# Performance work log

Measured on AMD Instinct MI355X. Metric: run time of the kernel, lower is better.

The kernel has to match this reference:

```python
import jax, jax.numpy as jnp
import numpy as np

S, B, D, H = 2048, 8, 512, 8
HD = D // H

def setup_inputs() -> dict:
    key = jax.random.key(0)
    ks = jax.random.split(key, 5)
    return {
        "src": jax.random.normal(ks[0], (S, B, D), dtype=jnp.float32),
        "in_proj_w": jax.random.normal(ks[1], (3 * D, D), dtype=jnp.float32) * (D ** -0.5),
        "in_proj_b": jax.random.normal(ks[2], (3 * D,), dtype=jnp.float32) * 0.02,
        "out_w": jax.random.normal(ks[3], (D, D), dtype=jnp.float32) * (D ** -0.5),
        "out_b": jax.random.normal(ks[4], (D,), dtype=jnp.float32) * 0.02,
    }

def reference(src, in_proj_w, in_proj_b, out_w, out_b):
    s, b, d = src.shape
    h, hd = H, HD
    # packed qkv projection: [S,B,3D]
    qkv = src @ in_proj_w.T + in_proj_b
    q, k, v = jnp.split(qkv, 3, axis=-1)
    # [S,B,H,hd]
    q = q.reshape(s, b, h, hd) * (hd ** -0.5)
    k = k.reshape(s, b, h, hd)
    v = v.reshape(s, b, h, hd)
    # scores [B,H,S,S]
    scores = jnp.einsum("sbhd,tbhd->bhst", q, k)
    attn = jax.nn.softmax(scores, axis=-1)
    # context [S,B,D]
    ctx = jnp.einsum("bhst,tbhd->sbhd", attn, v).reshape(s, b, d)
    out = ctx @ out_w.T + out_b
    # torch averages attention weights over heads when need_weights=True
    attn_weights = attn.mean(axis=1)  # [B,S,S]
    return out, attn_weights
```

## Files before the change

kernel.cpp:

```cpp
#include <hip/hip_runtime.h>
#include <hip/hip_bf16.h>

#define S_LEN 2048
#define BATCH 8
#define DMODEL 512
#define NHEAD 8
#define HDIM 64

#define QSCALE 0.18033688011112042f

typedef unsigned short u16;
typedef __bf16 bf16_t;
typedef bf16_t bf16x8 __attribute__((ext_vector_type(8)));
typedef float f32x4 __attribute__((ext_vector_type(4)));
typedef float f32x16 __attribute__((ext_vector_type(16)));
typedef u16 u16x8 __attribute__((ext_vector_type(8)));
typedef u16 u16x4 __attribute__((ext_vector_type(4)));
typedef unsigned u32x4 __attribute__((ext_vector_type(4)));

__device__ __forceinline__ u16 f2bf(float f) {
    unsigned u = __float_as_uint(f);
    u = (u + 0x7fffu + ((u >> 16) & 1u)) >> 16;
    return (u16)u;
}

__device__ __forceinline__ bf16x8 ld_frag(const u16* p) {
    u16x8 v = *(const u16x8*)p;
    return __builtin_bit_cast(bf16x8, v);
}

#define MFMA16(a, b, c) __builtin_amdgcn_mfma_f32_16x16x32_bf16((a), (b), (c), 0, 0, 0)
#define MFMA32(a, b, c) __builtin_amdgcn_mfma_f32_32x32x16_bf16((a), (b), (c), 0, 0, 0)
#define EXP2F(x) __builtin_amdgcn_exp2f(x)

__device__ __forceinline__ unsigned cvtpk(float lo, float hi) {
    unsigned r;
    asm("v_cvt_pk_bf16_f32 %0, %1, %2" : "=v"(r) : "v"(lo), "v"(hi));
    return r;
}
__device__ __forceinline__ void swap32(unsigned& a, unsigned& b) {
    asm("v_permlane32_swap_b32 %0, %1" : "+v"(a), "+v"(b));
}

__global__ __launch_bounds__(256) void cast_weights(const float* __restrict__ wq,
                                                    const float* __restrict__ wo,
                                                    u16* __restrict__ dst) {
    int i = (blockIdx.x * 256 + threadIdx.x) * 4;
    float4 v;
    if (i < 786432) v = *(const float4*)(wq + i);
    else            v = *(const float4*)(wo + (i - 786432));
    u16x4 o = {f2bf(v.x), f2bf(v.y), f2bf(v.z), f2bf(v.w)};
    *(u16x4*)(dst + i) = o;
}

__global__ __launch_bounds__(256) void qkv_gemm(const float* __restrict__ src,
                                                const u16* __restrict__ Wq,
                                                const float* __restrict__ bias,
                                                u16* __restrict__ Qs,
                                                u16* __restrict__ Ks,
                                                u16* __restrict__ Vs) {
    __shared__ u16 Al[128][40];
    __shared__ u16 Bl[128][40];
    const int tid = threadIdx.x;
    const int lane = tid & 63, wid = tid >> 6;
    const int m0 = blockIdx.y * 128, n0 = blockIdx.x * 128;
    const int lr = lane & 15, lkg = lane >> 4, lk = lkg * 8;
    const int wr = (wid >> 1) * 64, wc = (wid & 1) * 64;
    const int ar = tid >> 1, ac = (tid & 1) * 16;

    f32x4 acc[4][4];
#pragma unroll
    for (int i = 0; i < 4; i++)
#pragma unroll
        for (int n = 0; n < 4; n++) acc[i][n] = (f32x4){0.f, 0.f, 0.f, 0.f};

    for (int k0 = 0; k0 < DMODEL; k0 += 32) {
        __syncthreads();
        {
            const float* sp = src + (size_t)(m0 + ar) * DMODEL + k0 + ac;
            float4 v0 = *(const float4*)(sp + 0);
            float4 v1 = *(const float4*)(sp + 4);
            float4 v2 = *(const float4*)(sp + 8);
            float4 v3 = *(const float4*)(sp + 12);
            u16x8 p0 = {f2bf(v0.x), f2bf(v0.y), f2bf(v0.z), f2bf(v0.w),
                        f2bf(v1.x), f2bf(v1.y), f2bf(v1.z), f2bf(v1.w)};
            u16x8 p1 = {f2bf(v2.x), f2bf(v2.y), f2bf(v2.z), f2bf(v2.w),
                        f2bf(v3.x), f2bf(v3.y), f2bf(v3.z), f2bf(v3.w)};
            *(u16x8*)&Al[ar][ac] = p0;
            *(u16x8*)&Al[ar][ac + 8] = p1;
            const u16* wp = Wq + (size_t)(n0 + ar) * DMODEL + k0 + ac;
            *(u16x8*)&Bl[ar][ac] = *(const u16x8*)wp;
            *(u16x8*)&Bl[ar][ac + 8] = *(const u16x8*)(wp + 8);
        }
        __syncthreads();
        bf16x8 af[4], bfr[4];
#pragma unroll
        for (int i = 0; i < 4; i++) af[i] = ld_frag(&Al[wr + i * 16 + lr][lk]);
#pragma unroll
        for (int n = 0; n < 4; n++) bfr[n] = ld_frag(&Bl[wc + n * 16 + lr][lk]);
#pragma unroll
        for (int i = 0; i < 4; i++)
#pragma unroll
            for (int n = 0; n < 4; n++) acc[i][n] = MFMA16(af[i], bfr[n], acc[i][n]);
    }

    float bv[4];
#pragma unroll
    for (int n = 0; n < 4; n++) bv[n] = bias[n0 + wc + n * 16 + lr];
#pragma unroll
    for (int i = 0; i < 4; i++) {
#pragma unroll
        for (int n = 0; n < 4; n++) {
            int ncol = n0 + wc + n * 16 + lr;
            int sect = ncol >> 9, idx = ncol & 511;
            int h = idx >> 6, d = idx & 63;
#pragma unroll
            for (int j = 0; j < 4; j++) {
                int m = m0 + wr + i * 16 + lkg * 4 + j;
                int srow = m >> 3, bidx = m & 7;
                float val = acc[i][n][j] + bv[n];
                size_t o = (((size_t)(bidx * NHEAD + h) * S_LEN) + srow) * HDIM + d;
                if (sect == 0)      Qs[o] = f2bf(val * QSCALE);
                else if (sect == 1) Ks[o] = f2bf(val);
                else                Vs[o] = f2bf(val);
            }
        }
    }
}

__global__ __launch_bounds__(256) void transpose_v(const u16* __restrict__ Vs,
                                                   u16* __restrict__ Vt) {
    __shared__ u16 tile[64][70];
    int bh = blockIdx.y, t0 = blockIdx.x * 64;
    int tid = threadIdx.x;
    int r = tid >> 2, c = (tid & 3) * 16;
    const u16* vp = Vs + ((size_t)bh * S_LEN + t0 + r) * HDIM + c;
    u16x8 x0 = *(const u16x8*)vp;
    u16x8 x1 = *(const u16x8*)(vp + 8);
#pragma unroll
    for (int i = 0; i < 8; i++) tile[r][c + i] = x0[i];
#pragma unroll
    for (int i = 0; i < 8; i++) tile[r][c + 8 + i] = x1[i];
    __syncthreads();
    int d0 = tid >> 2, tt = (tid & 3) * 16;
    u16x8 y0, y1;
#pragma unroll
    for (int i = 0; i < 8; i++) y0[i] = tile[tt + i][d0];
#pragma unroll
    for (int i = 0; i < 8; i++) y1[i] = tile[tt + 8 + i][d0];
    u16* op = Vt + ((size_t)bh * HDIM + d0) * S_LEN + t0 + tt;
    *(u16x8*)op = y0;
    *(u16x8*)(op + 8) = y1;
}

__global__ __launch_bounds__(256) void ctx_kernel(const u16* __restrict__ Qs,
                                                  const u16* __restrict__ Ks,
                                                  const u16* __restrict__ Vt,
                                                  float* __restrict__ Lr,
                                                  u16* __restrict__ Ctx) {
    __shared__ char lds[32768];
    __shared__ float cjl[4][32];
    const int tid = threadIdx.x, lane = tid & 63, wid = tid >> 6;
    const int l31 = lane & 31, hi = lane >> 5;
    const int bh = blockIdx.y, b = bh >> 3, h = bh & 7;
    const int q0w = blockIdx.x * 128 + wid * 32;
    const u16* Qb = Qs + (size_t)bh * S_LEN * HDIM;
    const u16* Kb = Ks + (size_t)bh * S_LEN * HDIM;
    const u16* Vb = Vt + (size_t)bh * HDIM * S_LEN;

    bf16x8 qf[4];
#pragma unroll
    for (int kc = 0; kc < 4; kc++)
        qf[kc] = ld_frag(Qb + (size_t)(q0w + l31) * HDIM + kc * 16 + hi * 8);

    const int o0 = tid * 32;
    const int srow = o0 >> 7, scol = o0 & 127;
    const int p0 = srow * 128 + (scol ^ ((srow & 7) << 4));
    const int p1 = srow * 128 + ((scol + 16) ^ ((srow & 7) << 4));
    const char* Ksrc = (const char*)Kb + (size_t)srow * 128 + scol;
    const char* Vsrc = (const char*)(Vb + (size_t)srow * S_LEN) + scol;

    u16x8 sreg0, sreg1, sreg2, sreg3;
    sreg0 = *(const u16x8*)(Ksrc);
    sreg1 = *(const u16x8*)(Ksrc + 16);
    sreg2 = *(const u16x8*)(Vsrc);
    sreg3 = *(const u16x8*)(Vsrc + 16);
    *(u16x8*)(lds + p0) = sreg0;
    *(u16x8*)(lds + p1) = sreg1;
    *(u16x8*)(lds + 8192 + p0) = sreg2;
    *(u16x8*)(lds + 8192 + p1) = sreg3;
    __syncthreads();

    f32x16 cacc0, cacc1;
#pragma unroll
    for (int r = 0; r < 16; r++) { cacc0[r] = 0.f; cacc1[r] = 0.f; }
    float lsum = 0.f;
    int buf = 0;

    for (int it = 0; it < 32; ++it) {
        if (it < 31) {
            const char* kn = Ksrc + (size_t)(it + 1) * 8192;
            const char* vn = Vsrc + (size_t)(it + 1) * 128;
            sreg0 = *(const u16x8*)(kn);
            sreg1 = *(const u16x8*)(kn + 16);
            sreg2 = *(const u16x8*)(vn);
            sreg3 = *(const u16x8*)(vn + 16);
        }
        const char* Kl = lds + buf * 16384;
        const char* Vl = Kl + 8192;

        f32x16 st0, st1;
#pragma unroll
        for (int r = 0; r < 16; r++) { st0[r] = 0.f; st1[r] = 0.f; }
        __builtin_amdgcn_s_setprio(1);
#pragma unroll
        for (int kc = 0; kc < 4; kc++) {
            int row0 = l31, row1 = 32 + l31;
            int c = kc * 32 + hi * 16;
            bf16x8 a0 = *(const bf16x8*)(Kl + row0 * 128 + (c ^ ((row0 & 7) << 4)));
            bf16x8 a1 = *(const bf16x8*)(Kl + row1 * 128 + (c ^ ((row1 & 7) << 4)));
            st0 = MFMA32(a0, qf[kc], st0);
            st1 = MFMA32(a1, qf[kc], st1);
        }
        __builtin_amdgcn_s_setprio(0);

#pragma unroll
        for (int r = 0; r < 16; r++) {
            float e0 = EXP2F(st0[r]);
            float e1 = EXP2F(st1[r]);
            lsum += e0 + e1;
            st0[r] = e0;
            st1[r] = e1;
        }

        bf16x8 pa[4];
#pragma unroll
        for (int half = 0; half < 2; half++) {
            int h8 = half * 8;
            unsigned a0 = cvtpk(st0[h8 + 0], st0[h8 + 1]);
            unsigned b0 = cvtpk(st0[h8 + 4], st0[h8 + 5]);
            swap32(a0, b0);
            unsigned a1 = cvtpk(st0[h8 + 2], st0[h8 + 3]);
            unsigned b1 = cvtpk(st0[h8 + 6], st0[h8 + 7]);
            swap32(a1, b1);
            u32x4 w = {a0, a1, b0, b1};
            pa[half] = __builtin_bit_cast(bf16x8, w);
        }
#pragma unroll
        for (int half = 0; half < 2; half++) {
            int h8 = half * 8;
            unsigned a0 = cvtpk(st1[h8 + 0], st1[h8 + 1]);
            unsigned b0 = cvtpk(st1[h8 + 4], st1[h8 + 5]);
            swap32(a0, b0);
            unsigned a1 = cvtpk(st1[h8 + 2], st1[h8 + 3]);
            unsigned b1 = cvtpk(st1[h8 + 6], st1[h8 + 7]);
            swap32(a1, b1);
            u32x4 w = {a0, a1, b0, b1};
            pa[2 + half] = __builtin_bit_cast(bf16x8, w);
        }

        __builtin_amdgcn_s_setprio(1);
#pragma unroll
        for (int ks = 0; ks < 4; ks++) {
            int c = ks * 32 + hi * 16;
            int row0 = l31, row1 = 32 + l31;
            bf16x8 v0 = *(const bf16x8*)(Vl + row0 * 128 + (c ^ ((row0 & 7) << 4)));
            bf16x8 v1 = *(const bf16x8*)(Vl + row1 * 128 + (c ^ ((row1 & 7) << 4)));
            cacc0 = MFMA32(pa[ks], v0, cacc0);
            cacc1 = MFMA32(pa[ks], v1, cacc1);
        }
        __builtin_amdgcn_s_setprio(0);

        if (it < 31) {
            char* d = lds + (buf ^ 1) * 16384;
            *(u16x8*)(d + p0) = sreg0;
            *(u16x8*)(d + p1) = sreg1;
            *(u16x8*)(d + 8192 + p0) = sreg2;
            *(u16x8*)(d + 8192 + p1) = sreg3;
        }
        __syncthreads();
        buf ^= 1;
    }

    float tot = lsum + __shfl_xor(lsum, 32);
    float cj = 1.0f / tot;
    if (hi == 0) {
        Lr[(size_t)bh * S_LEN + q0w + l31] = cj;
        cjl[wid][l31] = cj;
    }
    float cjr[16];
#pragma unroll
    for (int r = 0; r < 16; r++)
        cjr[r] = cjl[wid][(r & 3) + 8 * (r >> 2) + 4 * hi];

#pragma unroll
    for (int r = 0; r < 16; r++) {
        int q = q0w + (r & 3) + 8 * (r >> 2) + 4 * hi;
        size_t base = ((size_t)q * BATCH + b) * DMODEL + h * 64;
        Ctx[base + l31] = f2bf(cacc0[r] * cjr[r]);
        Ctx[base + 32 + l31] = f2bf(cacc1[r] * cjr[r]);
    }
}

__global__ __launch_bounds__(256) void mean_kernel(const u16* __restrict__ Qs,
                                                   const u16* __restrict__ Ks,
                                                   const float* __restrict__ Lr,
                                                   float* __restrict__ attnw) {
    __shared__ char lds[32768];
    const int b = blockIdx.y;
    const int r0 = (blockIdx.x & 15) * 128, t0 = (blockIdx.x >> 4) * 64;
    const int tid = threadIdx.x, lane = tid & 63, wid = tid >> 6;
    const int lr = lane & 15, lkg = lane >> 4;
    const int swz = (lr & 7) << 4;
    const int qrow0 = r0 + wid * 32;

    const int o0 = tid * 32;
    const int srow = o0 >> 7, scol = o0 & 127;
    const int d0 = srow * 128 + (scol ^ ((srow & 7) << 4));
    const int d1 = srow * 128 + ((scol + 16) ^ ((srow & 7) << 4));

    f32x4 macc[2][4];
#pragma unroll
    for (int g = 0; g < 2; g++)
#pragma unroll
        for (int n = 0; n < 4; n++) macc[g][n] = (f32x4){0.f, 0.f, 0.f, 0.f};

    for (int rd = 0; rd < 2; ++rd) {
        if (rd) __syncthreads();
#pragma unroll
        for (int h = 0; h < 4; ++h) {
            const char* kp = (const char*)(Ks +
                (size_t)((b * NHEAD + rd * 4 + h) * S_LEN + t0) * HDIM) + o0;
            u16x8 c0 = *(const u16x8*)kp;
            u16x8 c1 = *(const u16x8*)(kp + 16);
            char* dst = lds + h * 8192;
            *(u16x8*)(dst + d0) = c0;
            *(u16x8*)(dst + d1) = c1;
        }
        __syncthreads();
#pragma unroll
        for (int h = 0; h < 4; ++h) {
            const int bh = b * NHEAD + rd * 4 + h;
            const u16* Qb = Qs + (size_t)bh * S_LEN * HDIM;
            const char* Kl = lds + h * 8192;

            bf16x8 bb0[4], bb1[4];
#pragma unroll
            for (int n = 0; n < 4; n++) {
                int row = n * 16 + lr;
                bb0[n] = *(const bf16x8*)(Kl + row * 128 + ((lkg * 16) ^ swz));
                bb1[n] = *(const bf16x8*)(Kl + row * 128 + ((64 + lkg * 16) ^ swz));
            }
            f32x4 cj0 = 0.125f * *(const f32x4*)(Lr + (size_t)bh * S_LEN + qrow0 + lkg * 4);
            f32x4 cj1 = 0.125f * *(const f32x4*)(Lr + (size_t)bh * S_LEN + qrow0 + 16 + lkg * 4);

            {
                bf16x8 a0 = ld_frag(Qb + (size_t)(qrow0 + lr) * HDIM + lkg * 8);
                bf16x8 a1 = ld_frag(Qb + (size_t)(qrow0 + lr) * HDIM + 32 + lkg * 8);
                f32x4 sc[4];
#pragma unroll
                for (int n = 0; n < 4; n++) sc[n] = (f32x4){0.f, 0.f, 0.f, 0.f};
#pragma unroll
                for (int n = 0; n < 4; n++) {
                    sc[n] = MFMA16(a0, bb0[n], sc[n]);
                    sc[n] = MFMA16(a1, bb1[n], sc[n]);
                }
#pragma unroll
                for (int n = 0; n < 4; n++)
#pragma unroll
                    for (int j = 0; j < 4; j++)
                        macc[0][n][j] += EXP2F(sc[n][j]) * cj0[j];
            }
            {
                bf16x8 a0 = ld_frag(Qb + (size_t)(qrow0 + 16 + lr) * HDIM + lkg * 8);
                bf16x8 a1 = ld_frag(Qb + (size_t)(qrow0 + 16 + lr) * HDIM + 32 + lkg * 8);
                f32x4 sc[4];
#pragma unroll
                for (int n = 0; n < 4; n++) sc[n] = (f32x4){0.f, 0.f, 0.f, 0.f};
#pragma unroll
                for (int n = 0; n < 4; n++) {
                    sc[n] = MFMA16(a0, bb0[n], sc[n]);
                    sc[n] = MFMA16(a1, bb1[n], sc[n]);
                }
#pragma unroll
                for (int n = 0; n < 4; n++)
#pragma unroll
                    for (int j = 0; j < 4; j++)
                        macc[1][n][j] += EXP2F(sc[n][j]) * cj1[j];
            }
        }
    }

#pragma unroll
    for (int g = 0; g < 2; g++)
#pragma unroll
        for (int n = 0; n < 4; n++)
#pragma unroll
            for (int j = 0; j < 4; j++) {
                int row = qrow0 + g * 16 + lkg * 4 + j;
                attnw[((size_t)b * S_LEN + row) * S_LEN + t0 + n * 16 + lr] =
                    macc[g][n][j];
            }
}

__global__ __launch_bounds__(256) void out_gemm(const u16* __restrict__ Ctx,
                                                const u16* __restrict__ Wo,
                                                const float* __restrict__ obias,
                                                float* __restrict__ out) {
    __shared__ u16 Al[128][40];
    __shared__ u16 Bl[128][40];
    const int tid = threadIdx.x;
    const int lane = tid & 63, wid = tid >> 6;
    const int m0 = blockIdx.y * 128, n0 = blockIdx.x * 128;
    const int lr = lane & 15, lkg = lane >> 4, lk = lkg * 8;
    const int wr = (wid >> 1) * 64, wc = (wid & 1) * 64;
    const int ar = tid >> 1, ac = (tid & 1) * 16;

    f32x4 acc[4][4];
#pragma unroll
    for (int i = 0; i < 4; i++)
#pragma unroll
        for (int n = 0; n < 4; n++) acc[i][n] = (f32x4){0.f, 0.f, 0.f, 0.f};

    for (int k0 = 0; k0 < DMODEL; k0 += 32) {
        __syncthreads();
        {
            const u16* apz = Ctx + (size_t)(m0 + ar) * DMODEL + k0 + ac;
            *(u16x8*)&Al[ar][ac] = *(const u16x8*)apz;
            *(u16x8*)&Al[ar][ac + 8] = *(const u16x8*)(apz + 8);
            const u16* wp = Wo + (size_t)(n0 + ar) * DMODEL + k0 + ac;
            *(u16x8*)&Bl[ar][ac] = *(const u16x8*)wp;
            *(u16x8*)&Bl[ar][ac + 8] = *(const u16x8*)(wp + 8);
        }
        __syncthreads();
        bf16x8 af[4], bfr[4];
#pragma unroll
        for (int i = 0; i < 4; i++) af[i] = ld_frag(&Al[wr + i * 16 + lr][lk]);
#pragma unroll
        for (int n = 0; n < 4; n++) bfr[n] = ld_frag(&Bl[wc + n * 16 + lr][lk]);
#pragma unroll
        for (int i = 0; i < 4; i++)
#pragma unroll
            for (int n = 0; n < 4; n++) acc[i][n] = MFMA16(af[i], bfr[n], acc[i][n]);
    }

    float bv[4];
#pragma unroll
    for (int n = 0; n < 4; n++) bv[n] = obias[n0 + wc + n * 16 + lr];
#pragma unroll
    for (int i = 0; i < 4; i++)
#pragma unroll
        for (int n = 0; n < 4; n++) {
            int ncol = n0 + wc + n * 16 + lr;
#pragma unroll
            for (int j = 0; j < 4; j++) {
                int m = m0 + wr + i * 16 + lkg * 4 + j;
                out[(size_t)m * DMODEL + ncol] = acc[i][n][j] + bv[n];
            }
        }
}

extern "C" void kernel_launch(void* const* d_in, const int* in_sizes, int n_in,
                              void* d_out, int out_size, void* d_ws, size_t ws_size,
                              hipStream_t stream) {
    const float* src   = (const float*)d_in[0];
    const float* w_in  = (const float*)d_in[1];
    const float* b_in  = (const float*)d_in[2];
    const float* w_out = (const float*)d_in[3];
    const float* b_out = (const float*)d_in[4];
    float* out = (float*)d_out;
    float* attnw = out + (size_t)S_LEN * BATCH * DMODEL;

    float* Lr = (float*)d_ws;
    u16* Wqb = (u16*)(Lr + 131072);
    u16* Wob = Wqb + 786432;
    u16* Qs  = Wob + 262144;
    u16* Ks  = Qs + 8388608;
    u16* Vs  = Ks + 8388608;
    u16* Vt  = Vs + 8388608;
    u16* Ctx = Vt + 8388608;

    cast_weights<<<dim3(1024), dim3(256), 0, stream>>>(w_in, w_out, Wqb);
    qkv_gemm<<<dim3(12, 128), dim3(256), 0, stream>>>(src, Wqb, b_in, Qs, Ks, Vs);
    transpose_v<<<dim3(32, 64), dim3(256), 0, stream>>>(Vs, Vt);
    ctx_kernel<<<dim3(16, 64), dim3(256), 0, stream>>>(Qs, Ks, Vt, Lr, Ctx);
    mean_kernel<<<dim3(512, 8), dim3(256), 0, stream>>>(Qs, Ks, Lr, attnw);
    out_gemm<<<dim3(4, 128), dim3(256), 0, stream>>>(Ctx, Wob, b_out, out);
}
```

Measured before the change: 461.4 us.

## Pre-cast src to bf16 once and double-buffer K tiles in mean kernel

The fp32 source is now converted to bf16 once in the cast kernel, so the QKV GEMM no longer re-reads and re-converts src in each of its 12 column blocks. The mean kernel now stages K two heads at a time into a double-buffered LDS area, prefetching the next pair into registers while computing the current one. It also interleaves both query groups per K fragment and adds a launch-bounds occupancy hint. The cost is an extra 16 MB bf16 buffer write/read, and the fused loop carries more live registers.

```diff
diff --git a/kernel.cpp b/kernel.cpp
--- a/kernel.cpp
+++ b/kernel.cpp
@@ -32,6 +32,7 @@
 #define MFMA16(a, b, c) __builtin_amdgcn_mfma_f32_16x16x32_bf16((a), (b), (c), 0, 0, 0)
 #define MFMA32(a, b, c) __builtin_amdgcn_mfma_f32_32x32x16_bf16((a), (b), (c), 0, 0, 0)
 #define EXP2F(x) __builtin_amdgcn_exp2f(x)
+#define ZERO4 ((f32x4){0.f, 0.f, 0.f, 0.f})
 
 __device__ __forceinline__ unsigned cvtpk(float lo, float hi) {
     unsigned r;
@@ -42,18 +43,20 @@
     asm("v_permlane32_swap_b32 %0, %1" : "+v"(a), "+v"(b));
 }
 
-__global__ __launch_bounds__(256) void cast_weights(const float* __restrict__ wq,
-                                                    const float* __restrict__ wo,
-                                                    u16* __restrict__ dst) {
+__global__ __launch_bounds__(256) void cast_inputs(const float* __restrict__ src,
+                                                   const float* __restrict__ wq,
+                                                   const float* __restrict__ wo,
+                                                   u16* __restrict__ dst) {
     int i = (blockIdx.x * 256 + threadIdx.x) * 4;
     float4 v;
-    if (i < 786432) v = *(const float4*)(wq + i);
-    else            v = *(const float4*)(wo + (i - 786432));
+    if (i < 8388608)      v = *(const float4*)(src + i);
+    else if (i < 9175040) v = *(const float4*)(wq + (i - 8388608));
+    else                  v = *(const float4*)(wo + (i - 9175040));
     u16x4 o = {f2bf(v.x), f2bf(v.y), f2bf(v.z), f2bf(v.w)};
     *(u16x4*)(dst + i) = o;
 }
 
-__global__ __launch_bounds__(256) void qkv_gemm(const float* __restrict__ src,
+__global__ __launch_bounds__(256) void qkv_gemm(const u16* __restrict__ srcb,
                                                 const u16* __restrict__ Wq,
                                                 const float* __restrict__ bias,
                                                 u16* __restrict__ Qs,
@@ -72,22 +75,14 @@
 #pragma unroll
     for (int i = 0; i < 4; i++)
 #pragma unroll
-        for (int n = 0; n < 4; n++) acc[i][n] = (f32x4){0.f, 0.f, 0.f, 0.f};
+        for (int n = 0; n < 4; n++) acc[i][n] = ZERO4;
 
     for (int k0 = 0; k0 < DMODEL; k0 += 32) {
         __syncthreads();
         {
-            const float* sp = src + (size_t)(m0 + ar) * DMODEL + k0 + ac;
-            float4 v0 = *(const float4*)(sp + 0);
-            float4 v1 = *(const float4*)(sp + 4);
-            float4 v2 = *(const float4*)(sp + 8);
-            float4 v3 = *(const float4*)(sp + 12);
-            u16x8 p0 = {f2bf(v0.x), f2bf(v0.y), f2bf(v0.z), f2bf(v0.w),
-                        f2bf(v1.x), f2bf(v1.y), f2bf(v1.z), f2bf(v1.w)};
-            u16x8 p1 = {f2bf(v2.x), f2bf(v2.y), f2bf(v2.z), f2bf(v2.w),
-                        f2bf(v3.x), f2bf(v3.y), f2bf(v3.z), f2bf(v3.w)};
-            *(u16x8*)&Al[ar][ac] = p0;
-            *(u16x8*)&Al[ar][ac + 8] = p1;
+            const u16* sp = srcb + (size_t)(m0 + ar) * DMODEL + k0 + ac;
+            *(u16x8*)&Al[ar][ac] = *(const u16x8*)sp;
+            *(u16x8*)&Al[ar][ac + 8] = *(const u16x8*)(sp + 8);
             const u16* wp = Wq + (size_t)(n0 + ar) * DMODEL + k0 + ac;
             *(u16x8*)&Bl[ar][ac] = *(const u16x8*)wp;
             *(u16x8*)&Bl[ar][ac + 8] = *(const u16x8*)(wp + 8);
@@ -302,93 +297,91 @@
     }
 }
 
-__global__ __launch_bounds__(256) void mean_kernel(const u16* __restrict__ Qs,
-                                                   const u16* __restrict__ Ks,
-                                                   const float* __restrict__ Lr,
-                                                   float* __restrict__ attnw) {
+__global__ __launch_bounds__(256, 4) void mean_kernel(const u16* __restrict__ Qs,
+                                                      const u16* __restrict__ Ks,
+                                                      const float* __restrict__ Lr,
+                                                      float* __restrict__ attnw) {
     __shared__ char lds[32768];
     const int b = blockIdx.y;
     const int r0 = (blockIdx.x & 15) * 128, t0 = (blockIdx.x >> 4) * 64;
     const int tid = threadIdx.x, lane = tid & 63, wid = tid >> 6;
     const int lr = lane & 15, lkg = lane >> 4;
-    const int swz = (lr & 7) << 4;
     const int qrow0 = r0 + wid * 32;
 
     const int o0 = tid * 32;
     const int srow = o0 >> 7, scol = o0 & 127;
     const int d0 = srow * 128 + (scol ^ ((srow & 7) << 4));
     const int d1 = srow * 128 + ((scol + 16) ^ ((srow & 7) << 4));
+    const char* Kbase = (const char*)(Ks + ((size_t)(b * NHEAD) * S_LEN + t0) * HDIM) + o0;
+    const size_t hstep = (size_t)S_LEN * HDIM * sizeof(u16);
+
+    {
+        u16x8 c0 = *(const u16x8*)(Kbase);
+        u16x8 c1 = *(const u16x8*)(Kbase + 16);
+        u16x8 c2 = *(const u16x8*)(Kbase + hstep);
+        u16x8 c3 = *(const u16x8*)(Kbase + hstep + 16);
+        *(u16x8*)(lds + d0) = c0;
+        *(u16x8*)(lds + d1) = c1;
+        *(u16x8*)(lds + 8192 + d0) = c2;
+        *(u16x8*)(lds + 8192 + d1) = c3;
+    }
+    __syncthreads();
 
     f32x4 macc[2][4];
 #pragma unroll
     for (int g = 0; g < 2; g++)
 #pragma unroll
-        for (int n = 0; n < 4; n++) macc[g][n] = (f32x4){0.f, 0.f, 0.f, 0.f};
-
-    for (int rd = 0; rd < 2; ++rd) {
-        if (rd) __syncthreads();
-#pragma unroll
-        for (int h = 0; h < 4; ++h) {
-            const char* kp = (const char*)(Ks +
-                (size_t)((b * NHEAD + rd * 4 + h) * S_LEN + t0) * HDIM) + o0;
-            u16x8 c0 = *(const u16x8*)kp;
-            u16x8 c1 = *(const u16x8*)(kp + 16);
-            char* dst = lds + h * 8192;
-            *(u16x8*)(dst + d0) = c0;
-            *(u16x8*)(dst + d1) = c1;
-        }
-        __syncthreads();
-#pragma unroll
-        for (int h = 0; h < 4; ++h) {
-            const int bh = b * NHEAD + rd * 4 + h;
+        for (int n = 0; n < 4; n++) macc[g][n] = ZERO4;
+
+    u16x8 nc0, nc1, nc2, nc3;
+    for (int p = 0; p < 4; ++p) {
+        if (p < 3) {
+            const char* k2 = Kbase + (size_t)(2 * p + 2) * hstep;
+            const char* k3 = Kbase + (size_t)(2 * p + 3) * hstep;
+            nc0 = *(const u16x8*)(k2);
+            nc1 = *(const u16x8*)(k2 + 16);
+            nc2 = *(const u16x8*)(k3);
+            nc3 = *(const u16x8*)(k3 + 16);
+        }
+        const char* bufA = lds + (p & 1) * 16384;
+#pragma unroll
+        for (int hh = 0; hh < 2; ++hh) {
+            const int bh = b * NHEAD + 2 * p + hh;
             const u16* Qb = Qs + (size_t)bh * S_LEN * HDIM;
-            const char* Kl = lds + h * 8192;
-
-            bf16x8 bb0[4], bb1[4];
-#pragma unroll
-            for (int n = 0; n < 4; n++) {
-                int row = n * 16 + lr;
-                bb0[n] = *(const bf16x8*)(Kl + row * 128 + ((lkg * 16) ^ swz));
-                bb1[n] = *(const bf16x8*)(Kl + row * 128 + ((64 + lkg * 16) ^ swz));
-            }
+            const char* Kl = bufA + hh * 8192;
+
+            bf16x8 a0g0 = ld_frag(Qb + (size_t)(qrow0 + lr) * HDIM + lkg * 8);
+            bf16x8 a1g0 = ld_frag(Qb + (size_t)(qrow0 + lr) * HDIM + 32 + lkg * 8);
+            bf16x8 a0g1 = ld_frag(Qb + (size_t)(qrow0 + 16 + lr) * HDIM + lkg * 8);
+            bf16x8 a1g1 = ld_frag(Qb + (size_t)(qrow0 + 16 + lr) * HDIM + 32 + lkg * 8);
             f32x4 cj0 = 0.125f * *(const f32x4*)(Lr + (size_t)bh * S_LEN + qrow0 + lkg * 4);
             f32x4 cj1 = 0.125f * *(const f32x4*)(Lr + (size_t)bh * S_LEN + qrow0 + 16 + lkg * 4);
 
-            {
-                bf16x8 a0 = ld_frag(Qb + (size_t)(qrow0 + lr) * HDIM + lkg * 8);
-                bf16x8 a1 = ld_frag(Qb + (size_t)(qrow0 + lr) * HDIM + 32 + lkg * 8);
-                f32x4 sc[4];
-#pragma unroll
-                for (int n = 0; n < 4; n++) sc[n] = (f32x4){0.f, 0.f, 0.f, 0.f};
-#pragma unroll
-                for (int n = 0; n < 4; n++) {
-                    sc[n] = MFMA16(a0, bb0[n], sc[n]);
-                    sc[n] = MFMA16(a1, bb1[n], sc[n]);
+#pragma unroll
+            for (int n = 0; n < 4; ++n) {
+                int row = n * 16 + lr;
+                int cbase = row * 128, sw = (row & 7) << 4;
+                bf16x8 kb0 = *(const bf16x8*)(Kl + cbase + ((lkg * 16) ^ sw));
+                bf16x8 kb1 = *(const bf16x8*)(Kl + cbase + ((64 + lkg * 16) ^ sw));
+                f32x4 s0 = MFMA16(a0g0, kb0, ZERO4);
+                s0 = MFMA16(a1g0, kb1, s0);
+                f32x4 s1 = MFMA16(a0g1, kb0, ZERO4);
+                s1 = MFMA16(a1g1, kb1, s1);
+#pragma unroll
+                for (int j = 0; j < 4; j++) {
+                    macc[0][n][j] += EXP2F(s0[j]) * cj0[j];
+                    macc[1][n][j] += EXP2F(s1[j]) * cj1[j];
                 }
-#pragma unroll
-                for (int n = 0; n < 4; n++)
-#pragma unroll
-                    for (int j = 0; j < 4; j++)
-                        macc[0][n][j] += EXP2F(sc[n][j]) * cj0[j];
             }
-            {
-                bf16x8 a0 = ld_frag(Qb + (size_t)(qrow0 + 16 + lr) * HDIM + lkg * 8);
-                bf16x8 a1 = ld_frag(Qb + (size_t)(qrow0 + 16 + lr) * HDIM + 32 + lkg * 8);
-                f32x4 sc[4];
-#pragma unroll
-                for (int n = 0; n < 4; n++) sc[n] = (f32x4){0.f, 0.f, 0.f, 0.f};
-#pragma unroll
-                for (int n = 0; n < 4; n++) {
-                    sc[n] = MFMA16(a0, bb0[n], sc[n]);
-                    sc[n] = MFMA16(a1, bb1[n], sc[n]);
-                }
-#pragma unroll
-                for (int n = 0; n < 4; n++)
-#pragma unroll
-                    for (int j = 0; j < 4; j++)
-                        macc[1][n][j] += EXP2F(sc[n][j]) * cj1[j];
-            }
-        }
+        }
+        if (p < 3) {
+            char* dB = lds + (((p & 1) ^ 1)) * 16384;
+            *(u16x8*)(dB + d0) = nc0;
+            *(u16x8*)(dB + d1) = nc1;
+            *(u16x8*)(dB + 8192 + d0) = nc2;
+            *(u16x8*)(dB + 8192 + d1) = nc3;
+        }
+        __syncthreads();
     }
 
 #pragma unroll
@@ -420,7 +413,7 @@
 #pragma unroll
     for (int i = 0; i < 4; i++)
 #pragma unroll
-        for (int n = 0; n < 4; n++) acc[i][n] = (f32x4){0.f, 0.f, 0.f, 0.f};
+        for (int n = 0; n < 4; n++) acc[i][n] = ZERO4;
 
     for (int k0 = 0; k0 < DMODEL; k0 += 32) {
         __syncthreads();
@@ -472,16 +465,17 @@
     float* attnw = out + (size_t)S_LEN * BATCH * DMODEL;
 
     float* Lr = (float*)d_ws;
-    u16* Wqb = (u16*)(Lr + 131072);
-    u16* Wob = Wqb + 786432;
-    u16* Qs  = Wob + 262144;
-    u16* Ks  = Qs + 8388608;
-    u16* Vs  = Ks + 8388608;
-    u16* Vt  = Vs + 8388608;
-    u16* Ctx = Vt + 8388608;
-
-    cast_weights<<<dim3(1024), dim3(256), 0, stream>>>(w_in, w_out, Wqb);
-    qkv_gemm<<<dim3(12, 128), dim3(256), 0, stream>>>(src, Wqb, b_in, Qs, Ks, Vs);
+    u16* Srcb = (u16*)(Lr + 131072);
+    u16* Wqb  = Srcb + 8388608;
+    u16* Wob  = Wqb + 786432;
+    u16* Qs   = Wob + 262144;
+    u16* Ks   = Qs + 8388608;
+    u16* Vs   = Ks + 8388608;
+    u16* Vt   = Vs + 8388608;
+    u16* Ctx  = Vt + 8388608;
+
+    cast_inputs<<<dim3(9216), dim3(256), 0, stream>>>(src, w_in, w_out, Srcb);
+    qkv_gemm<<<dim3(12, 128), dim3(256), 0, stream>>>(Srcb, Wqb, b_in, Qs, Ks, Vs);
     transpose_v<<<dim3(32, 64), dim3(256), 0, stream>>>(Vs, Vt);
     ctx_kernel<<<dim3(16, 64), dim3(256), 0, stream>>>(Qs, Ks, Vt, Lr, Ctx);
     mean_kernel<<<dim3(512, 8), dim3(256), 0, stream>>>(Qs, Ks, Lr, attnw);
```

Measured after the change: 510.1 us. +10.5%, slower.
